# Kernel optimization log

Measured on AMD Instinct MI355X. Metric: run time of the kernel, lower is better.

## Reference

```python
import jax, jax.numpy as jnp
import numpy as np

T, B, H, L = 200, 32, 1024, 2
DROPOUT = 0.32
KEEP = 1.0 - DROPOUT
FORGET_GATE_BIAS = 1.0


def setup_inputs() -> dict:
    key = jax.random.key(0)
    ks = jax.random.split(key, 8)
    scale = 1.0 / np.sqrt(H)  # torch LSTM default init: U(-1/sqrt(H), 1/sqrt(H))
    x = jax.random.normal(ks[0], (T, B, H), jnp.float32)
    W_ih = jax.random.uniform(ks[1], (L, 4 * H, H), jnp.float32, -scale, scale)
    W_hh = jax.random.uniform(ks[2], (L, 4 * H, H), jnp.float32, -scale, scale)
    b_ih = jax.random.uniform(ks[3], (L, 4 * H), jnp.float32, -scale, scale)
    b_hh = jax.random.uniform(ks[4], (L, 4 * H), jnp.float32, -scale, scale)
    # forget-gate bias init as in LstmDrop.__init__ (gate order i,f,g,o)
    b_ih = b_ih.at[:, H:2 * H].set(FORGET_GATE_BIAS)
    b_hh = b_hh.at[:, H:2 * H].set(0.0)
    h0 = jnp.zeros((L, B, H), jnp.float32)
    c0 = jnp.zeros((L, B, H), jnp.float32)
    # inverted dropout masks: inter-layer (torch LSTM dropout, applied to all but last layer)
    # and the trailing inplace Dropout on the output sequence
    mask_inter = (jax.random.bernoulli(ks[5], KEEP, (L - 1, T, B, H)) / KEEP).astype(jnp.float32)
    mask_out = (jax.random.bernoulli(ks[6], KEEP, (T, B, H)) / KEEP).astype(jnp.float32)
    return {"x": x, "h0": h0, "c0": c0, "W_ih": W_ih, "W_hh": W_hh,
            "b_ih": b_ih, "b_hh": b_hh, "mask_inter": mask_inter, "mask_out": mask_out}


def _lstm_layer(xs, h, c, Wih, Whh, b):
    # xs: [T,B,in]; Wih/Whh: [4H,in]/[4H,H]; b: [4H] (b_ih + b_hh fused)
    def step(carry, x_t):
        h, c = carry
        gates = x_t @ Wih.T + h @ Whh.T + b  # [B,4H]
        i, f, g, o = jnp.split(gates, 4, axis=-1)
        c = jax.nn.sigmoid(f) * c + jax.nn.sigmoid(i) * jnp.tanh(g)
        h = jax.nn.sigmoid(o) * jnp.tanh(c)
        return (h, c), h
    (hT, cT), ys = jax.lax.scan(step, (h, c), xs)
    return ys, hT, cT


def reference(x, h0, c0, W_ih, W_hh, b_ih, b_hh, mask_inter, mask_out):
    y = x
    h_last, c_last = [], []
    for l in range(L):
        y, hT, cT = _lstm_layer(y, h0[l], c0[l], W_ih[l], W_hh[l], b_ih[l] + b_hh[l])
        h_last.append(hT)
        c_last.append(cT)
        if l < L - 1:  # torch LSTM applies dropout between layers only
            y = y * mask_inter[l]
    y = y * mask_out  # the inplace Dropout on the output sequence
    return y, jnp.stack(h_last), jnp.stack(c_last)
```

## Files before the change

kernel.cpp:

```cpp
#include <hip/hip_runtime.h>

#define T_STEPS 200
#define BATCH   32
#define HID     1024
#define NWG     256
#define NTHR    512

typedef _Float16 half8 __attribute__((ext_vector_type(8)));
typedef float    f32x4 __attribute__((ext_vector_type(4)));

struct Bar {
    unsigned cnt[8 * 32];
    unsigned gcnt;
    unsigned pad[31];
    unsigned gen;
};

__device__ __forceinline__ half8 ld_coh16(const _Float16* p) {
    union { unsigned long long u[2]; half8 h; } r;
    const unsigned long long* q = (const unsigned long long*)p;
    r.u[0] = __hip_atomic_load(q,     __ATOMIC_RELAXED, __HIP_MEMORY_SCOPE_AGENT);
    r.u[1] = __hip_atomic_load(q + 1, __ATOMIC_RELAXED, __HIP_MEMORY_SCOPE_AGENT);
    return r.h;
}
__device__ __forceinline__ void st_coh16(_Float16* p, half8 v) {
    union { half8 h; unsigned long long u[2]; } r; r.h = v;
    unsigned long long* q = (unsigned long long*)p;
    __hip_atomic_store(q,     r.u[0], __ATOMIC_RELAXED, __HIP_MEMORY_SCOPE_AGENT);
    __hip_atomic_store(q + 1, r.u[1], __ATOMIC_RELAXED, __HIP_MEMORY_SCOPE_AGENT);
}

__global__ void init_k(const float* __restrict__ h0,
                       _Float16* __restrict__ h0b, _Float16* __restrict__ h1b,
                       Bar* __restrict__ bar) {
    int i = blockIdx.x * blockDim.x + threadIdx.x;
    if (i < BATCH * HID) {
        h0b[i] = (_Float16)h0[i];
        h1b[i] = (_Float16)h0[BATCH * HID + i];
    }
    if (i == 0) {
        for (int g = 0; g < 8; ++g) bar->cnt[g * 32] = 0;
        bar->gcnt = 0;
        bar->gen  = 0;
    }
}

__global__ __launch_bounds__(NTHR, 2) void lstm_main(
    const float* __restrict__ x, const float* __restrict__ c0,
    const float* __restrict__ Wih, const float* __restrict__ Whh,
    const float* __restrict__ bih, const float* __restrict__ bhh,
    const float* __restrict__ mi, const float* __restrict__ mo,
    float* __restrict__ out,
    _Float16* __restrict__ y0m, _Float16* __restrict__ h0b,
    _Float16* __restrict__ h1b, Bar* __restrict__ bar)
{
    __shared__ _Float16 W_s[32 * 2048];
    __shared__ float scr[8][2][16][17];
    __shared__ float c_s[BATCH][8];
    __shared__ alignas(16) _Float16 st_h[BATCH][8];
    __shared__ alignas(16) _Float16 st_y[BATCH][8];

    const int bid   = blockIdx.x;
    const int layer = bid >> 7;
    const int wgl   = bid & 127;
    const int tid   = threadIdx.x;

    const float* WihL = Wih + (size_t)layer * 4 * HID * HID;
    const float* WhhL = Whh + (size_t)layer * 4 * HID * HID;
    for (int idx = tid; idx < 32 * 2048; idx += NTHR) {
        int r = idx >> 11, k = idx & 2047;
        int grow = (r >> 3) * HID + wgl * 8 + (r & 7);
        float v = (k < HID) ? WihL[(size_t)grow * HID + k]
                            : WhhL[(size_t)grow * HID + (k - HID)];
        W_s[idx ^ ((r & 7) << 3)] = (_Float16)v;
    }

    float bias0 = 0.f, bias1 = 0.f, bias2 = 0.f, bias3 = 0.f;
    int b_ = 0, col_ = 0, gcol = 0;
    if (tid < 256) {
        b_ = tid >> 3; col_ = tid & 7; gcol = wgl * 8 + col_;
        bias0 = bih[layer * 4096 + gcol]           + bhh[layer * 4096 + gcol];
        bias1 = bih[layer * 4096 + HID + gcol]     + bhh[layer * 4096 + HID + gcol];
        bias2 = bih[layer * 4096 + 2 * HID + gcol] + bhh[layer * 4096 + 2 * HID + gcol];
        bias3 = bih[layer * 4096 + 3 * HID + gcol] + bhh[layer * 4096 + 3 * HID + gcol];
        c_s[b_][col_] = c0[((size_t)layer * BATCH + b_) * HID + gcol];
    }
    __syncthreads();

    const int lane = tid & 63, wid = tid >> 6;
    const int m  = wid & 1;
    const int kq = wid >> 1;
    const int row = lane & 15, bb = m * 16 + row, ko = (lane >> 4) * 8;
    const int grp = bid & 7;

    for (int tk = 0; tk <= T_STEPS; ++tk) {
        const bool active = (layer == 0) ? (tk < T_STEPS) : (tk >= 1);
        if (active) {
            const int t = (layer == 0) ? tk : tk - 1;
            const _Float16* hrd = (layer == 0) ? (h0b + (tk & 1) * (BATCH * HID))
                                               : (h1b + (((tk + 1) & 1)) * (BATCH * HID));
            f32x4 acc0 = {0.f, 0.f, 0.f, 0.f}, acc1 = {0.f, 0.f, 0.f, 0.f};

            half8 aF[16];
            if (kq < 2) {
                if (layer == 0) {
                    const float* xp = x + ((size_t)t * BATCH + bb) * HID + kq * 512 + ko;
                    #pragma unroll
                    for (int kk = 0; kk < 16; ++kk) {
                        f32x4 lo = *(const f32x4*)(xp + kk * 32);
                        f32x4 hi = *(const f32x4*)(xp + kk * 32 + 4);
                        half8 a;
                        a[0] = (_Float16)lo[0]; a[1] = (_Float16)lo[1];
                        a[2] = (_Float16)lo[2]; a[3] = (_Float16)lo[3];
                        a[4] = (_Float16)hi[0]; a[5] = (_Float16)hi[1];
                        a[6] = (_Float16)hi[2]; a[7] = (_Float16)hi[3];
                        aF[kk] = a;
                    }
                } else {
                    const _Float16* yp = y0m + ((size_t)t * BATCH + bb) * HID + kq * 512 + ko;
                    #pragma unroll
                    for (int kk = 0; kk < 16; ++kk) aF[kk] = ld_coh16(yp + kk * 32);
                }
            } else {
                const _Float16* hp = hrd + bb * HID + (kq - 2) * 512 + ko;
                #pragma unroll
                for (int kk = 0; kk < 16; ++kk) aF[kk] = ld_coh16(hp + kk * 32);
            }

            #pragma unroll
            for (int kk = 0; kk < 16; ++kk) {
                const int k  = kq * 512 + kk * 32 + ko;
                const int r1 = 16 + row;
                const half8 b0 = *(const half8*)&W_s[(row * 2048 + k) ^ ((row & 7) << 3)];
                const half8 b1 = *(const half8*)&W_s[(r1 * 2048 + k) ^ ((r1 & 7) << 3)];
                acc0 = __builtin_amdgcn_mfma_f32_16x16x32_f16(aF[kk], b0, acc0, 0, 0, 0);
                acc1 = __builtin_amdgcn_mfma_f32_16x16x32_f16(aF[kk], b1, acc1, 0, 0, 0);
            }
            #pragma unroll
            for (int j = 0; j < 4; ++j) {
                scr[wid][0][(lane >> 4) * 4 + j][row] = acc0[j];
                scr[wid][1][(lane >> 4) * 4 + j][row] = acc1[j];
            }
            __syncthreads();

            if (tid < 256) {
                const int m2 = b_ >> 4, rD = b_ & 15;
                float v0 = 0.f, v1 = 0.f, v2 = 0.f, v3 = 0.f;
                #pragma unroll
                for (int q = 0; q < 4; ++q) {
                    v0 += scr[q * 2 + m2][0][rD][col_];
                    v1 += scr[q * 2 + m2][0][rD][8 + col_];
                    v2 += scr[q * 2 + m2][1][rD][col_];
                    v3 += scr[q * 2 + m2][1][rD][8 + col_];
                }
                const float ig = 1.f / (1.f + __expf(-(v0 + bias0)));
                const float fg = 1.f / (1.f + __expf(-(v1 + bias1)));
                const float gg = tanhf(v2 + bias2);
                const float og = 1.f / (1.f + __expf(-(v3 + bias3)));
                const float cc = fg * c_s[b_][col_] + ig * gg;
                const float hh = og * tanhf(cc);
                c_s[b_][col_] = cc;

                st_h[b_][col_] = (_Float16)hh;

                const size_t oidx = ((size_t)t * BATCH + b_) * HID + gcol;
                if (layer == 0) {
                    st_y[b_][col_] = (_Float16)(hh * mi[oidx]);
                } else {
                    out[oidx] = hh * mo[oidx];
                }
                if (t == T_STEPS - 1) {
                    const size_t base = (size_t)T_STEPS * BATCH * HID;
                    out[base + ((size_t)layer * BATCH + b_) * HID + gcol] = hh;
                    out[base + (size_t)2 * BATCH * HID + ((size_t)layer * BATCH + b_) * HID + gcol] = cc;
                }
            }
            __syncthreads();

            if (tid < BATCH) {
                _Float16* hwr = (layer == 0) ? (h0b + (((tk + 1) & 1)) * (BATCH * HID))
                                             : (h1b + ((tk & 1)) * (BATCH * HID));
                st_coh16(&hwr[tid * HID + wgl * 8], *(const half8*)st_h[tid]);
                if (layer == 0)
                    st_coh16(&y0m[((size_t)t * BATCH + tid) * HID + wgl * 8],
                             *(const half8*)st_y[tid]);
            }
        }

        if (tid == 0) {
            asm volatile("s_waitcnt vmcnt(0)" ::: "memory");
            const unsigned tgt = (unsigned)(tk + 1);
            bool fin = false;
            unsigned old = __hip_atomic_fetch_add(&bar->cnt[grp * 32], 1u,
                                                  __ATOMIC_RELAXED, __HIP_MEMORY_SCOPE_AGENT);
            if (old == 31u) {
                unsigned o2 = __hip_atomic_fetch_add(&bar->gcnt, 1u,
                                                     __ATOMIC_RELAXED, __HIP_MEMORY_SCOPE_AGENT);
                if (o2 == 7u) {
                    for (int g = 0; g < 8; ++g)
                        __hip_atomic_store(&bar->cnt[g * 32], 0u,
                                           __ATOMIC_RELAXED, __HIP_MEMORY_SCOPE_AGENT);
                    __hip_atomic_store(&bar->gcnt, 0u,
                                       __ATOMIC_RELAXED, __HIP_MEMORY_SCOPE_AGENT);
                    asm volatile("s_waitcnt vmcnt(0)" ::: "memory");
                    __hip_atomic_store(&bar->gen, tgt,
                                       __ATOMIC_RELAXED, __HIP_MEMORY_SCOPE_AGENT);
                    fin = true;
                }
            }
            if (!fin) {
                while (__hip_atomic_load(&bar->gen, __ATOMIC_RELAXED,
                                         __HIP_MEMORY_SCOPE_AGENT) < tgt)
                    __builtin_amdgcn_s_sleep(1);
            }
            asm volatile("" ::: "memory");
        }
        __syncthreads();
    }
}

extern "C" void kernel_launch(void* const* d_in, const int* in_sizes, int n_in,
                              void* d_out, int out_size, void* d_ws, size_t ws_size,
                              hipStream_t stream) {
    const float* x   = (const float*)d_in[0];
    const float* h0  = (const float*)d_in[1];
    const float* c0  = (const float*)d_in[2];
    const float* Wih = (const float*)d_in[3];
    const float* Whh = (const float*)d_in[4];
    const float* bih = (const float*)d_in[5];
    const float* bhh = (const float*)d_in[6];
    const float* mi  = (const float*)d_in[7];
    const float* mo  = (const float*)d_in[8];
    float* out = (float*)d_out;

    char* w = (char*)d_ws;
    _Float16* y0m = (_Float16*)w;
    _Float16* h0b = (_Float16*)(w + 13107200);
    _Float16* h1b = (_Float16*)(w + 13107200 + 131072);
    Bar*      bar = (Bar*)(w + 13107200 + 262144);

    hipLaunchKernelGGL(init_k, dim3(128), dim3(256), 0, stream, h0, h0b, h1b, bar);

    void* args[] = {(void*)&x, (void*)&c0, (void*)&Wih, (void*)&Whh,
                    (void*)&bih, (void*)&bhh, (void*)&mi, (void*)&mo,
                    (void*)&out, (void*)&y0m, (void*)&h0b, (void*)&h1b, (void*)&bar};
    hipLaunchCooperativeKernel((void*)lstm_main, dim3(NWG), dim3(NTHR),
                               args, 0, stream);
}
```

Measured before the change: 2.248 ms.

## Replace atomic-counter grid barrier with flag barrier and prefetch next-step inputs

The grid barrier no longer uses two-level atomic counters. Each workgroup now writes its own padded flag, block 0 polls all flags and then releases eight padded generation words, and each of the other blocks polls its group's word. While waiting at the barrier, layer-0 blocks prefetch and convert the next step's x slice and dropout mask into registers, and layer-1 blocks prefetch the output mask. This takes atomic RMW contention and input load latency off the serial per-step critical path. In exchange it adds a central polling block and keeps aF live in registers across the loop, which may raise register pressure.

```diff
diff --git a/kernel.cpp b/kernel.cpp
--- a/kernel.cpp
+++ b/kernel.cpp
@@ -10,10 +10,8 @@
 typedef float    f32x4 __attribute__((ext_vector_type(4)));
 
 struct Bar {
-    unsigned cnt[8 * 32];
-    unsigned gcnt;
-    unsigned pad[31];
-    unsigned gen;
+    unsigned flag[NWG * 32];
+    unsigned gen[8 * 32];
 };
 
 __device__ __forceinline__ half8 ld_coh16(const _Float16* p) {
@@ -28,6 +26,17 @@
     unsigned long long* q = (unsigned long long*)p;
     __hip_atomic_store(q,     r.u[0], __ATOMIC_RELAXED, __HIP_MEMORY_SCOPE_AGENT);
     __hip_atomic_store(q + 1, r.u[1], __ATOMIC_RELAXED, __HIP_MEMORY_SCOPE_AGENT);
+}
+
+__device__ __forceinline__ half8 cvt8(const float* p) {
+    f32x4 lo = *(const f32x4*)p;
+    f32x4 hi = *(const f32x4*)(p + 4);
+    half8 a;
+    a[0] = (_Float16)lo[0]; a[1] = (_Float16)lo[1];
+    a[2] = (_Float16)lo[2]; a[3] = (_Float16)lo[3];
+    a[4] = (_Float16)hi[0]; a[5] = (_Float16)hi[1];
+    a[6] = (_Float16)hi[2]; a[7] = (_Float16)hi[3];
+    return a;
 }
 
 __global__ void init_k(const float* __restrict__ h0,
@@ -38,10 +47,9 @@
         h0b[i] = (_Float16)h0[i];
         h1b[i] = (_Float16)h0[BATCH * HID + i];
     }
-    if (i == 0) {
-        for (int g = 0; g < 8; ++g) bar->cnt[g * 32] = 0;
-        bar->gcnt = 0;
-        bar->gen  = 0;
+    if (blockIdx.x == 0) {
+        if (threadIdx.x < NWG) bar->flag[threadIdx.x * 32] = 0;
+        if (threadIdx.x < 8)   bar->gen[threadIdx.x * 32]  = 0;
     }
 }
 
@@ -93,40 +101,42 @@
     const int row = lane & 15, bb = m * 16 + row, ko = (lane >> 4) * 8;
     const int grp = bid & 7;
 
+    half8 aF[16];
+    float mi_reg = 0.f, mo_reg = 0.f;
+    if (layer == 0) {
+        if (kq < 2) {
+            const float* xp = x + (size_t)bb * HID + kq * 512 + ko;
+            #pragma unroll
+            for (int kk = 0; kk < 16; ++kk) aF[kk] = cvt8(xp + kk * 32);
+        }
+        if (tid < 256) mi_reg = mi[(size_t)b_ * HID + gcol];
+    }
+
     for (int tk = 0; tk <= T_STEPS; ++tk) {
         const bool active = (layer == 0) ? (tk < T_STEPS) : (tk >= 1);
         if (active) {
             const int t = (layer == 0) ? tk : tk - 1;
-            const _Float16* hrd = (layer == 0) ? (h0b + (tk & 1) * (BATCH * HID))
-                                               : (h1b + (((tk + 1) & 1)) * (BATCH * HID));
-            f32x4 acc0 = {0.f, 0.f, 0.f, 0.f}, acc1 = {0.f, 0.f, 0.f, 0.f};
-
-            half8 aF[16];
-            if (kq < 2) {
-                if (layer == 0) {
-                    const float* xp = x + ((size_t)t * BATCH + bb) * HID + kq * 512 + ko;
+            if (layer == 0) {
+                if (kq >= 2) {
+                    const _Float16* hp = h0b + (tk & 1) * (BATCH * HID)
+                                       + bb * HID + (kq - 2) * 512 + ko;
                     #pragma unroll
-                    for (int kk = 0; kk < 16; ++kk) {
-                        f32x4 lo = *(const f32x4*)(xp + kk * 32);
-                        f32x4 hi = *(const f32x4*)(xp + kk * 32 + 4);
-                        half8 a;
-                        a[0] = (_Float16)lo[0]; a[1] = (_Float16)lo[1];
-                        a[2] = (_Float16)lo[2]; a[3] = (_Float16)lo[3];
-                        a[4] = (_Float16)hi[0]; a[5] = (_Float16)hi[1];
-                        a[6] = (_Float16)hi[2]; a[7] = (_Float16)hi[3];
-                        aF[kk] = a;
-                    }
-                } else {
+                    for (int kk = 0; kk < 16; ++kk) aF[kk] = ld_coh16(hp + kk * 32);
+                }
+            } else {
+                if (kq < 2) {
                     const _Float16* yp = y0m + ((size_t)t * BATCH + bb) * HID + kq * 512 + ko;
                     #pragma unroll
                     for (int kk = 0; kk < 16; ++kk) aF[kk] = ld_coh16(yp + kk * 32);
-                }
-            } else {
-                const _Float16* hp = hrd + bb * HID + (kq - 2) * 512 + ko;
-                #pragma unroll
-                for (int kk = 0; kk < 16; ++kk) aF[kk] = ld_coh16(hp + kk * 32);
-            }
-
+                } else {
+                    const _Float16* hp = h1b + (((tk + 1) & 1)) * (BATCH * HID)
+                                       + bb * HID + (kq - 2) * 512 + ko;
+                    #pragma unroll
+                    for (int kk = 0; kk < 16; ++kk) aF[kk] = ld_coh16(hp + kk * 32);
+                }
+            }
+
+            f32x4 acc0 = {0.f, 0.f, 0.f, 0.f}, acc1 = {0.f, 0.f, 0.f, 0.f};
             #pragma unroll
             for (int kk = 0; kk < 16; ++kk) {
                 const int k  = kq * 512 + kk * 32 + ko;
@@ -165,9 +175,9 @@
 
                 const size_t oidx = ((size_t)t * BATCH + b_) * HID + gcol;
                 if (layer == 0) {
-                    st_y[b_][col_] = (_Float16)(hh * mi[oidx]);
+                    st_y[b_][col_] = (_Float16)(hh * mi_reg);
                 } else {
-                    out[oidx] = hh * mo[oidx];
+                    out[oidx] = hh * mo_reg;
                 }
                 if (t == T_STEPS - 1) {
                     const size_t base = (size_t)T_STEPS * BATCH * HID;
@@ -187,34 +197,47 @@
             }
         }
 
+        if (tk == T_STEPS) break;
+
+        const unsigned tgt = (unsigned)(tk + 1);
+
         if (tid == 0) {
             asm volatile("s_waitcnt vmcnt(0)" ::: "memory");
-            const unsigned tgt = (unsigned)(tk + 1);
-            bool fin = false;
-            unsigned old = __hip_atomic_fetch_add(&bar->cnt[grp * 32], 1u,
-                                                  __ATOMIC_RELAXED, __HIP_MEMORY_SCOPE_AGENT);
-            if (old == 31u) {
-                unsigned o2 = __hip_atomic_fetch_add(&bar->gcnt, 1u,
-                                                     __ATOMIC_RELAXED, __HIP_MEMORY_SCOPE_AGENT);
-                if (o2 == 7u) {
-                    for (int g = 0; g < 8; ++g)
-                        __hip_atomic_store(&bar->cnt[g * 32], 0u,
-                                           __ATOMIC_RELAXED, __HIP_MEMORY_SCOPE_AGENT);
-                    __hip_atomic_store(&bar->gcnt, 0u,
-                                       __ATOMIC_RELAXED, __HIP_MEMORY_SCOPE_AGENT);
-                    asm volatile("s_waitcnt vmcnt(0)" ::: "memory");
-                    __hip_atomic_store(&bar->gen, tgt,
-                                       __ATOMIC_RELAXED, __HIP_MEMORY_SCOPE_AGENT);
-                    fin = true;
-                }
-            }
-            if (!fin) {
-                while (__hip_atomic_load(&bar->gen, __ATOMIC_RELAXED,
+            __hip_atomic_store(&bar->flag[bid * 32], tgt,
+                               __ATOMIC_RELAXED, __HIP_MEMORY_SCOPE_AGENT);
+        }
+
+        if (layer == 0) {
+            if (kq < 2 && tk + 1 < T_STEPS) {
+                const float* xp = x + ((size_t)(tk + 1) * BATCH + bb) * HID + kq * 512 + ko;
+                #pragma unroll
+                for (int kk = 0; kk < 16; ++kk) aF[kk] = cvt8(xp + kk * 32);
+            }
+            if (tid < 256 && tk + 1 < T_STEPS)
+                mi_reg = mi[((size_t)(tk + 1) * BATCH + b_) * HID + gcol];
+        } else {
+            if (tid < 256 && tk < T_STEPS)
+                mo_reg = mo[((size_t)tk * BATCH + b_) * HID + gcol];
+        }
+
+        if (bid == 0) {
+            if (tid < NWG) {
+                while (__hip_atomic_load(&bar->flag[tid * 32], __ATOMIC_RELAXED,
                                          __HIP_MEMORY_SCOPE_AGENT) < tgt)
                     __builtin_amdgcn_s_sleep(1);
             }
-            asm volatile("" ::: "memory");
-        }
+            __syncthreads();
+            if (tid < 8)
+                __hip_atomic_store(&bar->gen[tid * 32], tgt,
+                                   __ATOMIC_RELAXED, __HIP_MEMORY_SCOPE_AGENT);
+        } else {
+            if (tid == 0) {
+                while (__hip_atomic_load(&bar->gen[grp * 32], __ATOMIC_RELAXED,
+                                         __HIP_MEMORY_SCOPE_AGENT) < tgt)
+                    __builtin_amdgcn_s_sleep(1);
+            }
+        }
+        asm volatile("" ::: "memory");
         __syncthreads();
     }
 }
```

Result: slower. 2.452 ms (+9.1%).

## Rework grid barrier with parity counters, per-group gen flags, and LDS release spin

Applied to the files above, without the earlier changes.

Replaces the single-thread grid barrier with double-buffered (parity) arrival counters and eight padded generation flags, one per group, so waiters poll separate cache lines. The last arriver resets counters and publishes the generation in parallel across lanes instead of serially. Non-leader waves spin on an LDS flag with dummy FMAs instead of sitting in s_barrier, and the final barrier iteration is skipped. This adds complexity and busy-spinning waves that compete for issue slots in exchange for lower barrier latency per step.

```diff
diff --git a/kernel.cpp b/kernel.cpp
--- a/kernel.cpp
+++ b/kernel.cpp
@@ -10,10 +10,9 @@
 typedef float    f32x4 __attribute__((ext_vector_type(4)));
 
 struct Bar {
-    unsigned cnt[8 * 32];
-    unsigned gcnt;
-    unsigned pad[31];
-    unsigned gen;
+    unsigned cnt[2][8 * 32];
+    unsigned gcnt[2 * 32];
+    unsigned gen[8 * 32];
 };
 
 __device__ __forceinline__ half8 ld_coh16(const _Float16* p) {
@@ -28,6 +27,17 @@
     unsigned long long* q = (unsigned long long*)p;
     __hip_atomic_store(q,     r.u[0], __ATOMIC_RELAXED, __HIP_MEMORY_SCOPE_AGENT);
     __hip_atomic_store(q + 1, r.u[1], __ATOMIC_RELAXED, __HIP_MEMORY_SCOPE_AGENT);
+}
+
+__device__ __forceinline__ half8 cvt8(const float* p) {
+    f32x4 lo = *(const f32x4*)p;
+    f32x4 hi = *(const f32x4*)(p + 4);
+    half8 a;
+    a[0] = (_Float16)lo[0]; a[1] = (_Float16)lo[1];
+    a[2] = (_Float16)lo[2]; a[3] = (_Float16)lo[3];
+    a[4] = (_Float16)hi[0]; a[5] = (_Float16)hi[1];
+    a[6] = (_Float16)hi[2]; a[7] = (_Float16)hi[3];
+    return a;
 }
 
 __global__ void init_k(const float* __restrict__ h0,
@@ -38,10 +48,13 @@
         h0b[i] = (_Float16)h0[i];
         h1b[i] = (_Float16)h0[BATCH * HID + i];
     }
-    if (i == 0) {
-        for (int g = 0; g < 8; ++g) bar->cnt[g * 32] = 0;
-        bar->gcnt = 0;
-        bar->gen  = 0;
+    if (blockIdx.x == 0) {
+        if (threadIdx.x < 8) {
+            bar->cnt[0][threadIdx.x * 32] = 0;
+            bar->cnt[1][threadIdx.x * 32] = 0;
+            bar->gen[threadIdx.x * 32]    = 0;
+        }
+        if (threadIdx.x < 2) bar->gcnt[threadIdx.x * 32] = 0;
     }
 }
 
@@ -59,11 +72,14 @@
     __shared__ float c_s[BATCH][8];
     __shared__ alignas(16) _Float16 st_h[BATCH][8];
     __shared__ alignas(16) _Float16 st_y[BATCH][8];
+    __shared__ unsigned rel_flag;
 
     const int bid   = blockIdx.x;
     const int layer = bid >> 7;
     const int wgl   = bid & 127;
     const int tid   = threadIdx.x;
+
+    if (tid == 0) rel_flag = 0;
 
     const float* WihL = Wih + (size_t)layer * 4 * HID * HID;
     const float* WhhL = Whh + (size_t)layer * 4 * HID * HID;
@@ -106,16 +122,7 @@
                 if (layer == 0) {
                     const float* xp = x + ((size_t)t * BATCH + bb) * HID + kq * 512 + ko;
                     #pragma unroll
-                    for (int kk = 0; kk < 16; ++kk) {
-                        f32x4 lo = *(const f32x4*)(xp + kk * 32);
-                        f32x4 hi = *(const f32x4*)(xp + kk * 32 + 4);
-                        half8 a;
-                        a[0] = (_Float16)lo[0]; a[1] = (_Float16)lo[1];
-                        a[2] = (_Float16)lo[2]; a[3] = (_Float16)lo[3];
-                        a[4] = (_Float16)hi[0]; a[5] = (_Float16)hi[1];
-                        a[6] = (_Float16)hi[2]; a[7] = (_Float16)hi[3];
-                        aF[kk] = a;
-                    }
+                    for (int kk = 0; kk < 16; ++kk) aF[kk] = cvt8(xp + kk * 32);
                 } else {
                     const _Float16* yp = y0m + ((size_t)t * BATCH + bb) * HID + kq * 512 + ko;
                     #pragma unroll
@@ -187,34 +194,64 @@
             }
         }
 
-        if (tid == 0) {
-            asm volatile("s_waitcnt vmcnt(0)" ::: "memory");
-            const unsigned tgt = (unsigned)(tk + 1);
-            bool fin = false;
-            unsigned old = __hip_atomic_fetch_add(&bar->cnt[grp * 32], 1u,
-                                                  __ATOMIC_RELAXED, __HIP_MEMORY_SCOPE_AGENT);
-            if (old == 31u) {
-                unsigned o2 = __hip_atomic_fetch_add(&bar->gcnt, 1u,
-                                                     __ATOMIC_RELAXED, __HIP_MEMORY_SCOPE_AGENT);
-                if (o2 == 7u) {
-                    for (int g = 0; g < 8; ++g)
-                        __hip_atomic_store(&bar->cnt[g * 32], 0u,
-                                           __ATOMIC_RELAXED, __HIP_MEMORY_SCOPE_AGENT);
-                    __hip_atomic_store(&bar->gcnt, 0u,
-                                       __ATOMIC_RELAXED, __HIP_MEMORY_SCOPE_AGENT);
-                    asm volatile("s_waitcnt vmcnt(0)" ::: "memory");
-                    __hip_atomic_store(&bar->gen, tgt,
-                                       __ATOMIC_RELAXED, __HIP_MEMORY_SCOPE_AGENT);
-                    fin = true;
-                }
-            }
-            if (!fin) {
-                while (__hip_atomic_load(&bar->gen, __ATOMIC_RELAXED,
-                                         __HIP_MEMORY_SCOPE_AGENT) < tgt)
-                    __builtin_amdgcn_s_sleep(1);
-            }
-            asm volatile("" ::: "memory");
+        if (tk == T_STEPS) break;
+
+        const unsigned tgt = (unsigned)(tk + 1);
+        const int p = tk & 1;
+
+        if (wid == 0) {
+            int pubi = 0;
+            if (lane == 0) {
+                asm volatile("s_waitcnt vmcnt(0)" ::: "memory");
+                unsigned old = __hip_atomic_fetch_add(&bar->cnt[p][grp * 32], 1u,
+                                   __ATOMIC_RELAXED, __HIP_MEMORY_SCOPE_AGENT);
+                if (old == 31u) {
+                    unsigned o2 = __hip_atomic_fetch_add(&bar->gcnt[p * 32], 1u,
+                                       __ATOMIC_RELAXED, __HIP_MEMORY_SCOPE_AGENT);
+                    pubi = (o2 == 7u) ? 1 : 0;
+                }
+            }
+            pubi = __shfl(pubi, 0);
+            if (pubi) {
+                if (lane < 8)
+                    __hip_atomic_store(&bar->gen[lane * 32], tgt,
+                                       __ATOMIC_RELAXED, __HIP_MEMORY_SCOPE_AGENT);
+                else if (lane < 16)
+                    __hip_atomic_store(&bar->cnt[p][(lane - 8) * 32], 0u,
+                                       __ATOMIC_RELAXED, __HIP_MEMORY_SCOPE_AGENT);
+                else if (lane == 16)
+                    __hip_atomic_store(&bar->gcnt[p * 32], 0u,
+                                       __ATOMIC_RELAXED, __HIP_MEMORY_SCOPE_AGENT);
+            }
+            if (lane == 0) {
+                if (!pubi) {
+                    float j0 = 0.f, j1 = 0.f;
+                    while (__hip_atomic_load(&bar->gen[grp * 32], __ATOMIC_RELAXED,
+                                             __HIP_MEMORY_SCOPE_AGENT) < tgt) {
+                        asm volatile("v_fma_f32 %0,%0,%0,%0\n"
+                                     "v_fma_f32 %1,%1,%1,%1\n"
+                                     "v_fma_f32 %0,%0,%0,%0\n"
+                                     "v_fma_f32 %1,%1,%1,%1"
+                                     : "+v"(j0), "+v"(j1));
+                    }
+                }
+                *(volatile unsigned*)&rel_flag = tgt;
+            }
+        } else {
+            float j0 = 0.f, j1 = 0.f, j2 = 0.f, j3 = 0.f;
+            while (*(volatile unsigned*)&rel_flag < tgt) {
+                asm volatile("v_fma_f32 %0,%0,%0,%0\n"
+                             "v_fma_f32 %1,%1,%1,%1\n"
+                             "v_fma_f32 %2,%2,%2,%2\n"
+                             "v_fma_f32 %3,%3,%3,%3\n"
+                             "v_fma_f32 %0,%0,%0,%0\n"
+                             "v_fma_f32 %1,%1,%1,%1\n"
+                             "v_fma_f32 %2,%2,%2,%2\n"
+                             "v_fma_f32 %3,%3,%3,%3"
+                             : "+v"(j0), "+v"(j1), "+v"(j2), "+v"(j3));
+            }
         }
+        asm volatile("" ::: "memory");
         __syncthreads();
     }
 }
```

Result: faster. 2.177 ms (-3.2%).
